# Kernel tuning notes

Measured on AMD Instinct MI355X. Metric: run time of the kernel, lower is better.

Reference implementation:

```python
import jax, jax.numpy as jnp
import numpy as np

P = 0.8
EPS = 1e-6


def setup_inputs() -> dict:
    key = jax.random.key(0)
    k1, k2 = jax.random.split(key)
    N, C = 8192, 2048
    logits = jax.random.normal(k1, (N, C), dtype=jnp.float32)
    labels = jax.random.randint(k2, (N,), 0, C, dtype=jnp.int64)
    return {"logits": logits, "labels": labels}


def reference(logits, labels):
    N, C = logits.shape
    # targets: one-hot class indicators, [N, C]
    targets = jax.nn.one_hot(labels, C, dtype=logits.dtype)
    # class counts (first-call behavior of the stateful module): sum over batch + 1
    class_counts = targets.sum(axis=0) + 1.0  # [C]
    # seesaw mitigation factor s[i, j] = (n_j / n_i)^p if n_i > n_j else 1
    ratio = class_counts[None, :] / class_counts[:, None]  # [C, C]
    s = jnp.where(class_counts[:, None] > class_counts[None, :], ratio ** P, 1.0)
    # stable exp
    logits = logits - logits.max(axis=-1, keepdims=True)
    e = jnp.exp(logits)  # [N, C]
    # denominator[n, i] = sum_j (1 - t[n,j]) * s[i,j] * e[n,j] + e[n,i]
    # == ((1 - t) * e) @ s.T + e  -- GEMM form of the O(N*C*C) broadcast-sum
    denom = jnp.einsum('nj,ij->ni', (1.0 - targets) * e, s) + e
    sigma = e / (denom + EPS)
    loss = (-targets * jnp.log(sigma + EPS)).sum(axis=-1)  # [N]
    return loss.mean()
```

## Files before the change

kernel.cpp:

```cpp
#include <hip/hip_runtime.h>
#include <math.h>

#define NROWS 8192
#define NCLS  2048
#define NBLK  1024
#define NTHR  512
#define LOG2E 1.44269504088896340736f
#define EPS   1e-6f


__global__ __launch_bounds__(512, 8) void seesaw_rows_k(
        const float* __restrict__ logits,
        const int*   __restrict__ labels,
        float*       __restrict__ part) {
    __shared__ __align__(16) int   cnt[NCLS];
    __shared__ __align__(16) float w[NCLS];
    __shared__ float red[8];

    const int t    = threadIdx.x;
    const int lane = t & 63;
    const int wid  = t >> 6;
    const int n    = blockIdx.x * 8 + wid;

    const int4* lab4 = reinterpret_cast<const int4*>(labels);
    int4 L0 = lab4[t];
    int4 L1 = lab4[t + 512];
    int4 L2 = lab4[t + 1024];
    int4 L3 = lab4[t + 1536];

    const int y = labels[n];

    const float4* r0 = reinterpret_cast<const float4*>(logits + (size_t)n * NCLS);
    float4 v[8];
    #pragma unroll
    for (int k = 0; k < 8; ++k) v[k] = r0[k * 64 + lane];

    const float ylogit = logits[(size_t)n * NCLS + y];

    reinterpret_cast<int4*>(cnt)[t] = make_int4(0, 0, 0, 0);
    asm volatile("s_waitcnt lgkmcnt(0)" ::: "memory");
    __builtin_amdgcn_s_barrier();
    asm volatile("" ::: "memory");

    atomicAdd(&cnt[L0.x], 1); atomicAdd(&cnt[L0.y], 1);
    atomicAdd(&cnt[L0.z], 1); atomicAdd(&cnt[L0.w], 1);
    atomicAdd(&cnt[L1.x], 1); atomicAdd(&cnt[L1.y], 1);
    atomicAdd(&cnt[L1.z], 1); atomicAdd(&cnt[L1.w], 1);
    atomicAdd(&cnt[L2.x], 1); atomicAdd(&cnt[L2.y], 1);
    atomicAdd(&cnt[L2.z], 1); atomicAdd(&cnt[L2.w], 1);
    atomicAdd(&cnt[L3.x], 1); atomicAdd(&cnt[L3.y], 1);
    atomicAdd(&cnt[L3.z], 1); atomicAdd(&cnt[L3.w], 1);
    asm volatile("s_waitcnt lgkmcnt(0)" ::: "memory");
    __builtin_amdgcn_s_barrier();
    asm volatile("" ::: "memory");

    #pragma unroll
    for (int j = t; j < NCLS; j += NTHR) w[j] = 0.8f * log2f((float)(cnt[j] + 1));
    asm volatile("s_waitcnt lgkmcnt(0)" ::: "memory");
    __builtin_amdgcn_s_barrier();
    asm volatile("" ::: "memory");

    const float4* wl4 = reinterpret_cast<const float4*>(w);
    const float wy = w[y];

    float sa = 0.0f, sb = 0.0f;
    #pragma unroll
    for (int k = 0; k < 8; ++k) {
        float4 wv = wl4[k * 64 + lane];
        sa += exp2f(fmaf(v[k].x, LOG2E, fminf(wv.x - wy, 0.0f)));
        sb += exp2f(fmaf(v[k].y, LOG2E, fminf(wv.y - wy, 0.0f)));
        sa += exp2f(fmaf(v[k].z, LOG2E, fminf(wv.z - wy, 0.0f)));
        sb += exp2f(fmaf(v[k].w, LOG2E, fminf(wv.w - wy, 0.0f)));
    }
    float s = sa + sb;
    #pragma unroll
    for (int off = 32; off; off >>= 1) s += __shfl_xor(s, off, 64);

    if (lane == 0) {
        float ey = exp2f(ylogit * LOG2E);
        red[wid] = -logf(ey / (s + EPS) + EPS);
    }
    __syncthreads();
    if (t == 0) {
        float bs = ((red[0] + red[1]) + (red[2] + red[3])) +
                   ((red[4] + red[5]) + (red[6] + red[7]));
        part[blockIdx.x] = bs;
    }
}

__global__ __launch_bounds__(256) void finalize_k(
        const float* __restrict__ part, float* __restrict__ out) {
    const int t = threadIdx.x, lane = t & 63, wid = t >> 6;
    const float4* p4 = reinterpret_cast<const float4*>(part);
    float4 v = p4[t];
    float s = (v.x + v.y) + (v.z + v.w);
    #pragma unroll
    for (int off = 32; off; off >>= 1) s += __shfl_xor(s, off, 64);
    __shared__ float red[4];
    if (lane == 0) red[wid] = s;
    __syncthreads();
    if (t == 0) out[0] = ((red[0] + red[1]) + (red[2] + red[3])) / (float)NROWS;
}

extern "C" void kernel_launch(void* const* d_in, const int* in_sizes, int n_in,
                              void* d_out, int out_size, void* d_ws, size_t ws_size,
                              hipStream_t stream) {
    const float* logits = (const float*)d_in[0];
    const int*   labels = (const int*)d_in[1];
    float* out  = (float*)d_out;
    float* part = (float*)d_ws;

    seesaw_rows_k<<<NBLK, NTHR, 0, stream>>>(logits, labels, part);
    finalize_k<<<1, 256, 0, stream>>>(part, out);
}
```

Baseline: 18.83 us.

## Fuse final reduction via two-level fixed-point atomic last-block accumulation

Removes the separate finalize kernel launch. Each block quantizes its partial loss to fixed point and atomically adds it, together with a packed arrival counter, into one of 32 group accumulators. The last block of each group forwards the group sum to a global accumulator, and the last group writes the mean. This adds a memset launch on the workspace and lowers the launch_bounds occupancy hint from 8 to 6. It also relies on the fixed-point scale and bias fitting without overflow.

```diff
diff --git a/kernel.cpp b/kernel.cpp
--- a/kernel.cpp
+++ b/kernel.cpp
@@ -7,12 +7,16 @@
 #define NTHR  512
 #define LOG2E 1.44269504088896340736f
 #define EPS   1e-6f
+#define QSC   1048576.0
+#define QBIAS (1ll << 30)
+#define CMASK ((1ull << 56) - 1)
 
 
-__global__ __launch_bounds__(512, 8) void seesaw_rows_k(
+__global__ __launch_bounds__(512, 6) void seesaw_all_k(
         const float* __restrict__ logits,
         const int*   __restrict__ labels,
-        float*       __restrict__ part) {
+        unsigned long long* __restrict__ acc,
+        float*       __restrict__ out) {
     __shared__ __align__(16) int   cnt[NCLS];
     __shared__ __align__(16) float w[NCLS];
     __shared__ float red[8];
@@ -81,25 +85,27 @@
         red[wid] = -logf(ey / (s + EPS) + EPS);
     }
     __syncthreads();
+
     if (t == 0) {
         float bs = ((red[0] + red[1]) + (red[2] + red[3])) +
                    ((red[4] + red[5]) + (red[6] + red[7]));
-        part[blockIdx.x] = bs;
+        unsigned long long q =
+            (unsigned long long)(llrint((double)bs * QSC) + QBIAS);
+        const int g = blockIdx.x >> 5;
+        unsigned long long* gline = acc + (size_t)g * 8;
+        unsigned long long old = atomicAdd(gline, (1ull << 56) | q);
+        if ((old >> 56) == 31ull) {
+            unsigned long long gtot = (old & CMASK) + q;
+            unsigned long long* fin = acc + 256;
+            unsigned long long o2 = atomicAdd(fin, (1ull << 56) | gtot);
+            if ((o2 >> 56) == 31ull) {
+                unsigned long long grand = (o2 & CMASK) + gtot;
+                double total = ((double)(long long)grand
+                               - (double)NBLK * (double)QBIAS) / QSC;
+                out[0] = (float)(total / (double)NROWS);
+            }
+        }
     }
-}
-
-__global__ __launch_bounds__(256) void finalize_k(
-        const float* __restrict__ part, float* __restrict__ out) {
-    const int t = threadIdx.x, lane = t & 63, wid = t >> 6;
-    const float4* p4 = reinterpret_cast<const float4*>(part);
-    float4 v = p4[t];
-    float s = (v.x + v.y) + (v.z + v.w);
-    #pragma unroll
-    for (int off = 32; off; off >>= 1) s += __shfl_xor(s, off, 64);
-    __shared__ float red[4];
-    if (lane == 0) red[wid] = s;
-    __syncthreads();
-    if (t == 0) out[0] = ((red[0] + red[1]) + (red[2] + red[3])) / (float)NROWS;
 }
 
 extern "C" void kernel_launch(void* const* d_in, const int* in_sizes, int n_in,
@@ -107,9 +113,9 @@
                               hipStream_t stream) {
     const float* logits = (const float*)d_in[0];
     const int*   labels = (const int*)d_in[1];
-    float* out  = (float*)d_out;
-    float* part = (float*)d_ws;
+    float* out = (float*)d_out;
+    unsigned long long* acc = (unsigned long long*)d_ws;
 
-    seesaw_rows_k<<<NBLK, NTHR, 0, stream>>>(logits, labels, part);
-    finalize_k<<<1, 256, 0, stream>>>(part, out);
+    hipMemsetAsync(d_ws, 0, 2112, stream);
+    seesaw_all_k<<<NBLK, NTHR, 0, stream>>>(logits, labels, acc, out);
 }
```

Result: slower. 22.65 us (+20.3%).
